# Kernel optimization log

Measured on AMD Instinct MI355X. Metric: run time of the kernel, lower is better.

The kernel has to match this reference:

```python
import jax, jax.numpy as jnp
import numpy as np

NUM_HEADS = 32
ROPE_THETA = 10000.0


def _apply_rope_neox(x, positions):
    # x: [B, S, H, D], positions: [B, S]
    D = x.shape[-1]
    inv_freq = 1.0 / (ROPE_THETA ** (jnp.arange(0, D, 2, dtype=jnp.float32) / D))  # [D/2]
    ang = positions.astype(jnp.float32)[..., None] * inv_freq  # [B, S, D/2]
    cos = jnp.cos(ang)[:, :, None, :]  # [B, S, 1, D/2]
    sin = jnp.sin(ang)[:, :, None, :]
    x1, x2 = x[..., : D // 2], x[..., D // 2 :]
    return jnp.concatenate([x1 * cos - x2 * sin, x2 * cos + x1 * sin], axis=-1)


def setup_inputs() -> dict:
    key = jax.random.key(0)
    ks = jax.random.split(key, 4)
    B, S, H = 2, 2048, 4096
    positions = jnp.broadcast_to(jnp.arange(S, dtype=jnp.int32), (B, S))
    hidden_states = jax.random.normal(ks[0], (B, S, H), dtype=jnp.float32)
    w_qkv = jax.random.normal(ks[1], (H, 3 * H), dtype=jnp.float32) * (H ** -0.5)
    b_qkv = jax.random.normal(ks[2], (3 * H,), dtype=jnp.float32) * 0.02
    w_proj = jax.random.normal(ks[3], (H, H), dtype=jnp.float32) * (H ** -0.5)
    return {"positions": positions, "hidden_states": hidden_states,
            "w_qkv": w_qkv, "b_qkv": b_qkv, "w_proj": w_proj}


def reference(positions, hidden_states, w_qkv, b_qkv, w_proj):
    B, S, H = hidden_states.shape
    nh = NUM_HEADS
    hd = H // nh
    scale = hd ** -0.5

    qkv = hidden_states @ w_qkv + b_qkv  # [B, S, 3H]
    q, k, v = jnp.split(qkv, 3, axis=-1)
    q = q.reshape(B, S, nh, hd)
    k = k.reshape(B, S, nh, hd)
    v = v.reshape(B, S, nh, hd)

    q = _apply_rope_neox(q, positions)
    k = _apply_rope_neox(k, positions)

    scores = jnp.einsum("bqhd,bkhd->bhqk", q, k) * scale  # [B, H, S, S]
    causal = jnp.tril(jnp.ones((S, S), dtype=bool))
    scores = jnp.where(causal, scores, jnp.finfo(scores.dtype).min)
    probs = jax.nn.softmax(scores, axis=-1)
    attn = jnp.einsum("bhqk,bkhd->bqhd", probs, v).reshape(B, S, H)

    return attn @ w_proj
```

## Files before the change

kernel.cpp:

```cpp
#include <hip/hip_runtime.h>

#define NHD 32
#define SS  2048
#define HH  4096
#define H3  12288
#define HD  128

typedef __attribute__((ext_vector_type(4))) float f32x4;
typedef __attribute__((ext_vector_type(8))) short short8;

#define GLOAD_LDS16(gptr, lptr)                                                        \
  __builtin_amdgcn_global_load_lds((const __attribute__((address_space(1))) void*)(gptr), \
                                   (__attribute__((address_space(3))) void*)(lptr), 16, 0, 0)

__device__ __forceinline__ ushort f2bf(float f) {
  union { float f; unsigned u; } v; v.f = f;
  unsigned r = (v.u + 0x7FFFu + ((v.u >> 16) & 1u)) >> 16;
  return (ushort)r;
}
__device__ __forceinline__ float bf2f(ushort u) {
  union { unsigned u; float f; } v; v.u = ((unsigned)u) << 16;
  return v.f;
}

__global__ __launch_bounds__(256) void cvt_f32_bf16(const float* __restrict__ in,
                                                    ushort* __restrict__ out) {
  size_t i = ((size_t)blockIdx.x * 256 + threadIdx.x) * 4;
  float4 v = *(const float4*)(in + i);
  ushort4 r; r.x = f2bf(v.x); r.y = f2bf(v.y); r.z = f2bf(v.z); r.w = f2bf(v.w);
  *(ushort4*)(out + i) = r;
}

__global__ __launch_bounds__(256) void transpose_cvt(const float* __restrict__ in,
                                                     ushort* __restrict__ out,
                                                     int rows, int cols) {
  __shared__ float tile[32][33];
  int c0 = blockIdx.x * 32, r0 = blockIdx.y * 32;
  int tx = threadIdx.x, ty = threadIdx.y;
  #pragma unroll
  for (int i = ty; i < 32; i += 8)
    tile[i][tx] = in[(size_t)(r0 + i) * cols + (c0 + tx)];
  __syncthreads();
  #pragma unroll
  for (int i = ty; i < 32; i += 8)
    out[(size_t)(c0 + i) * rows + (r0 + tx)] = f2bf(tile[tx][i]);
}

__global__ __launch_bounds__(256) void vtrans(const ushort* __restrict__ qkvb,
                                              ushort* __restrict__ vt) {
  __shared__ ushort tile[32][33];
  int s0 = blockIdx.x * 32, d0 = blockIdx.y * 32, bh = blockIdx.z;
  int b = bh >> 5, h = bh & 31;
  int tx = threadIdx.x, ty = threadIdx.y;
  #pragma unroll
  for (int i = ty; i < 32; i += 8)
    tile[i][tx] = qkvb[(size_t)(b * SS + s0 + i) * H3 + 8192 + h * 128 + d0 + tx];
  __syncthreads();
  #pragma unroll
  for (int i = ty; i < 32; i += 8)
    vt[((size_t)bh * HD + d0 + i) * SS + s0 + tx] = tile[tx][i];
}

template<bool BIAS, bool OUTBF16>
__global__ __launch_bounds__(256) void gemm_bf16(const ushort* __restrict__ A,
                                                 const ushort* __restrict__ BT,
                                                 const float* __restrict__ bias,
                                                 void* __restrict__ Cv,
                                                 int N, int K) {
  __shared__ __align__(16) ushort As[128 * 64];
  __shared__ __align__(16) ushort Bs[128 * 64];
  int tid  = threadIdx.x;
  int wave = tid >> 6, lane = tid & 63;
  int g = lane >> 4, q = lane & 15;
  int m0 = blockIdx.y * 128, n0 = blockIdx.x * 128;
  int wr = (wave >> 1) * 64, wc = (wave & 1) * 64;
  f32x4 acc[4][4] = {};
  for (int k0 = 0; k0 < K; k0 += 64) {
    __syncthreads();
    #pragma unroll
    for (int r = 0; r < 4; ++r) {
      int gr  = wave * 64 + 256 * r + lane;
      int row = gr >> 3, col = (gr & 7) << 3;
      int ldsbase = (wave * 64 + 256 * r) * 8;
      GLOAD_LDS16(A  + (size_t)(m0 + row) * K + k0 + col, &As[ldsbase]);
      GLOAD_LDS16(BT + (size_t)(n0 + row) * K + k0 + col, &Bs[ldsbase]);
    }
    __syncthreads();
    #pragma unroll
    for (int kk = 0; kk < 64; kk += 32) {
      short8 af[4], bfr[4];
      #pragma unroll
      for (int m = 0; m < 4; ++m)
        af[m] = *(const short8*)(&As[(wr + m * 16 + q) * 64 + kk + 8 * g]);
      #pragma unroll
      for (int n = 0; n < 4; ++n)
        bfr[n] = *(const short8*)(&Bs[(wc + n * 16 + q) * 64 + kk + 8 * g]);
      #pragma unroll
      for (int m = 0; m < 4; ++m)
        #pragma unroll
        for (int n = 0; n < 4; ++n)
          acc[m][n] = __builtin_amdgcn_mfma_f32_16x16x32_bf16(af[m], bfr[n], acc[m][n], 0, 0, 0);
    }
  }
  #pragma unroll
  for (int m = 0; m < 4; ++m) {
    #pragma unroll
    for (int n = 0; n < 4; ++n) {
      int gcol = n0 + wc + n * 16 + q;
      float bv = 0.f;
      if (BIAS) bv = bias[gcol];
      #pragma unroll
      for (int r = 0; r < 4; ++r) {
        int grow = m0 + wr + m * 16 + g * 4 + r;
        float v = acc[m][n][r] + bv;
        if (OUTBF16) ((ushort*)Cv)[(size_t)grow * N + gcol] = f2bf(v);
        else         ((float*) Cv)[(size_t)grow * N + gcol] = v;
      }
    }
  }
}

__global__ __launch_bounds__(256) void rope_split(const ushort* __restrict__ qkv,
                                                  const int* __restrict__ positions,
                                                  ushort* __restrict__ qb,
                                                  ushort* __restrict__ kb) {
  int id = blockIdx.x * 256 + threadIdx.x;
  int d = id & 63;
  int h = (id >> 6) & 31;
  int t = id >> 11;
  int b = t >> 11, s = t & 2047;
  float pos = (float)positions[t];
  float ang = pos * __expf(-(float)d * 0.14391156831212787f);
  float sv, cv;
  sincosf(ang, &sv, &cv);
  size_t src = (size_t)t * H3 + h * 128 + d;
  float q1 = bf2f(qkv[src]),        q2 = bf2f(qkv[src + 64]);
  float k1 = bf2f(qkv[src + 4096]), k2 = bf2f(qkv[src + 4160]);
  size_t dst = ((size_t)(b * NHD + h) * SS + s) * HD + d;
  qb[dst]      = f2bf(q1 * cv - q2 * sv);
  qb[dst + 64] = f2bf(q2 * cv + q1 * sv);
  kb[dst]      = f2bf(k1 * cv - k2 * sv);
  kb[dst + 64] = f2bf(k2 * cv + k1 * sv);
}

__global__ __launch_bounds__(256) void attn_fwd(const ushort* __restrict__ qb,
                                                const ushort* __restrict__ kb,
                                                const ushort* __restrict__ vt,
                                                ushort* __restrict__ aout) {
  __shared__ __align__(16) ushort Ks[64 * 128];
  __shared__ __align__(16) ushort Vs[128 * 64];
  __shared__ __align__(16) ushort Pw[4 * 32 * 68];
  const float SCALE = 0.08838834764831845f;
  int tid = threadIdx.x, wave = tid >> 6, lane = tid & 63;
  int g = lane >> 4, q = lane & 15;
  int swk = (q & 7) << 4;
  int bh = blockIdx.y;
  int qb0 = blockIdx.x * 128;
  const ushort* Qh = qb + (size_t)bh * SS * HD;
  const ushort* Kh = kb + (size_t)bh * SS * HD;
  const ushort* Vh = vt + (size_t)bh * SS * HD;
  ushort* Pm = &Pw[wave * 32 * 68];

  short8 qf[2][4];
  #pragma unroll
  for (int m = 0; m < 2; ++m)
    #pragma unroll
    for (int c = 0; c < 4; ++c)
      qf[m][c] = *(const short8*)(Qh + (size_t)(qb0 + wave * 32 + m * 16 + q) * HD + c * 32 + 8 * g);

  f32x4 o[2][8] = {};
  float mrow[2][4], lrow[2][4];
  #pragma unroll
  for (int m = 0; m < 2; ++m)
    #pragma unroll
    for (int r = 0; r < 4; ++r) { mrow[m][r] = -1e30f; lrow[m][r] = 0.f; }

  int nt = (qb0 >> 6) + 2;
  for (int kt = 0; kt < nt; ++kt) {
    int kv0 = kt * 64;
    __syncthreads();
    #pragma unroll
    for (int r = 0; r < 4; ++r) {
      int gi  = r * 256 + tid;
      int row = gi >> 4, xb = (gi & 15) << 4;
      int src = xb ^ ((row & 7) << 4);
      GLOAD_LDS16(Kh + (size_t)(kv0 + row) * HD + (src >> 1),
                  &Ks[(r * 256 + wave * 64) * 8]);
    }
    #pragma unroll
    for (int r = 0; r < 4; ++r) {
      int gi  = r * 256 + tid;
      int row = gi >> 3, xb = (gi & 7) << 4;
      int src = xb ^ ((row & 7) << 4);
      GLOAD_LDS16(Vh + (size_t)row * SS + kv0 + (src >> 1),
                  &Vs[(r * 256 + wave * 64) * 8]);
    }
    __syncthreads();

    f32x4 sf[2][4] = {};
    #pragma unroll
    for (int c = 0; c < 4; ++c) {
      #pragma unroll
      for (int n = 0; n < 4; ++n) {
        int row = n * 16 + q;
        short8 kf = *(const short8*)(&Ks[row * 128 + (((c * 64 + 16 * g) ^ swk) >> 1)]);
        #pragma unroll
        for (int m = 0; m < 2; ++m)
          sf[m][n] = __builtin_amdgcn_mfma_f32_16x16x32_bf16(qf[m][c], kf, sf[m][n], 0, 0, 0);
      }
    }

    bool masked = (kt >= nt - 2);
    float corr[2][4];
    #pragma unroll
    for (int m = 0; m < 2; ++m) {
      #pragma unroll
      for (int r = 0; r < 4; ++r) {
        int qrow = qb0 + wave * 32 + m * 16 + g * 4 + r;
        float x[4];
        #pragma unroll
        for (int n = 0; n < 4; ++n) {
          x[n] = sf[m][n][r] * SCALE;
          if (masked && (kv0 + n * 16 + q > qrow)) x[n] = -1e30f;
        }
        float mx = fmaxf(fmaxf(x[0], x[1]), fmaxf(x[2], x[3]));
        #pragma unroll
        for (int off = 8; off; off >>= 1) mx = fmaxf(mx, __shfl_xor(mx, off));
        float mnew = fmaxf(mrow[m][r], mx);
        corr[m][r] = __expf(mrow[m][r] - mnew);
        mrow[m][r] = mnew;
        float rs = 0.f;
        #pragma unroll
        for (int n = 0; n < 4; ++n) {
          float p = __expf(x[n] - mnew);
          rs += p;
          Pm[(m * 16 + g * 4 + r) * 68 + n * 16 + q] = f2bf(p);
        }
        #pragma unroll
        for (int off = 8; off; off >>= 1) rs += __shfl_xor(rs, off);
        lrow[m][r] = lrow[m][r] * corr[m][r] + rs;
      }
    }
    #pragma unroll
    for (int m = 0; m < 2; ++m)
      #pragma unroll
      for (int d0 = 0; d0 < 8; ++d0)
        #pragma unroll
        for (int r = 0; r < 4; ++r) o[m][d0][r] *= corr[m][r];

    short8 pf[2][2];
    #pragma unroll
    for (int m = 0; m < 2; ++m)
      #pragma unroll
      for (int c2 = 0; c2 < 2; ++c2)
        pf[m][c2] = *(const short8*)(&Pm[(m * 16 + q) * 68 + c2 * 32 + 8 * g]);
    #pragma unroll
    for (int d0 = 0; d0 < 8; ++d0) {
      int vrow = d0 * 16 + q;
      short8 vf0 = *(const short8*)(&Vs[vrow * 64 + (((16 * g) ^ swk) >> 1)]);
      short8 vf1 = *(const short8*)(&Vs[vrow * 64 + (((64 + 16 * g) ^ swk) >> 1)]);
      #pragma unroll
      for (int m = 0; m < 2; ++m) {
        o[m][d0] = __builtin_amdgcn_mfma_f32_16x16x32_bf16(pf[m][0], vf0, o[m][d0], 0, 0, 0);
        o[m][d0] = __builtin_amdgcn_mfma_f32_16x16x32_bf16(pf[m][1], vf1, o[m][d0], 0, 0, 0);
      }
    }
  }

  int b = bh >> 5, h = bh & 31;
  #pragma unroll
  for (int m = 0; m < 2; ++m) {
    #pragma unroll
    for (int r = 0; r < 4; ++r) {
      float inv = 1.0f / lrow[m][r];
      int srow = qb0 + wave * 32 + m * 16 + g * 4 + r;
      size_t base = ((size_t)(b * SS + srow)) * HH + h * 128;
      #pragma unroll
      for (int d0 = 0; d0 < 8; ++d0)
        aout[base + d0 * 16 + q] = f2bf(o[m][d0][r] * inv);
    }
  }
}

extern "C" void kernel_launch(void* const* d_in, const int* in_sizes, int n_in,
                              void* d_out, int out_size, void* d_ws, size_t ws_size,
                              hipStream_t stream) {
  const int*   positions = (const int*)  d_in[0];
  const float* hidden    = (const float*)d_in[1];
  const float* w_qkv     = (const float*)d_in[2];
  const float* b_qkv     = (const float*)d_in[3];
  const float* w_proj    = (const float*)d_in[4];
  float* out = (float*)d_out;

  char* ws = (char*)d_ws;
  ushort* hsb   = (ushort*)(ws);
  ushort* wqkvT = (ushort*)(ws + 0x02000000ULL);
  ushort* wpT   = (ushort*)(ws + 0x08000000ULL);
  ushort* qkvb  = (ushort*)(ws + 0x0A000000ULL);
  ushort* qbuf  = (ushort*)(ws + 0x10000000ULL);
  ushort* kbuf  = (ushort*)(ws + 0x12000000ULL);
  ushort* vtb   = (ushort*)(ws + 0x14000000ULL);
  ushort* aout  = hsb;

  cvt_f32_bf16<<<16384, 256, 0, stream>>>(hidden, hsb);
  transpose_cvt<<<dim3(384, 128), dim3(32, 8), 0, stream>>>(w_qkv, wqkvT, HH, H3);
  transpose_cvt<<<dim3(128, 128), dim3(32, 8), 0, stream>>>(w_proj, wpT, HH, HH);

  gemm_bf16<true, true><<<dim3(96, 32), 256, 0, stream>>>(hsb, wqkvT, b_qkv, qkvb, H3, HH);

  rope_split<<<32768, 256, 0, stream>>>(qkvb, positions, qbuf, kbuf);
  vtrans<<<dim3(64, 4, 64), dim3(32, 8), 0, stream>>>(qkvb, vtb);

  attn_fwd<<<dim3(16, 64), 256, 0, stream>>>(qbuf, kbuf, vtb, aout);

  gemm_bf16<false, false><<<dim3(32, 32), 256, 0, stream>>>(aout, wpT, nullptr, out, HH, HH);
}
```

Measured before the change: 1.744 ms.

## Replace GEMM with 256x256 double-buffered, swizzled, 8-wave pipelined kernel

Replaces the 128x128 single-buffered bf16 GEMM with a 256x256 tile kernel using 8 waves, double-buffered LDS, XOR-swizzled LDS layout, and interleaved async global-to-LDS loads with MFMA quadrants under raised wave priority. The aim is to hide global load latency behind MFMA work, avoid LDS bank conflicts, and raise arithmetic intensity per block. In exchange it uses 128KB of LDS per block and many more accumulator registers. The out-projection GEMM gets only 256 blocks, which may underfill the GPU.

```diff
diff --git a/kernel.cpp b/kernel.cpp
--- a/kernel.cpp
+++ b/kernel.cpp
@@ -62,57 +62,169 @@
 }
 
 template<bool BIAS, bool OUTBF16>
-__global__ __launch_bounds__(256) void gemm_bf16(const ushort* __restrict__ A,
-                                                 const ushort* __restrict__ BT,
-                                                 const float* __restrict__ bias,
-                                                 void* __restrict__ Cv,
-                                                 int N, int K) {
-  __shared__ __align__(16) ushort As[128 * 64];
-  __shared__ __align__(16) ushort Bs[128 * 64];
-  int tid  = threadIdx.x;
-  int wave = tid >> 6, lane = tid & 63;
-  int g = lane >> 4, q = lane & 15;
-  int m0 = blockIdx.y * 128, n0 = blockIdx.x * 128;
-  int wr = (wave >> 1) * 64, wc = (wave & 1) * 64;
-  f32x4 acc[4][4] = {};
-  for (int k0 = 0; k0 < K; k0 += 64) {
-    __syncthreads();
-    #pragma unroll
-    for (int r = 0; r < 4; ++r) {
-      int gr  = wave * 64 + 256 * r + lane;
-      int row = gr >> 3, col = (gr & 7) << 3;
-      int ldsbase = (wave * 64 + 256 * r) * 8;
-      GLOAD_LDS16(A  + (size_t)(m0 + row) * K + k0 + col, &As[ldsbase]);
-      GLOAD_LDS16(BT + (size_t)(n0 + row) * K + k0 + col, &Bs[ldsbase]);
-    }
-    __syncthreads();
-    #pragma unroll
-    for (int kk = 0; kk < 64; kk += 32) {
-      short8 af[4], bfr[4];
-      #pragma unroll
-      for (int m = 0; m < 4; ++m)
-        af[m] = *(const short8*)(&As[(wr + m * 16 + q) * 64 + kk + 8 * g]);
-      #pragma unroll
-      for (int n = 0; n < 4; ++n)
-        bfr[n] = *(const short8*)(&Bs[(wc + n * 16 + q) * 64 + kk + 8 * g]);
-      #pragma unroll
-      for (int m = 0; m < 4; ++m)
-        #pragma unroll
-        for (int n = 0; n < 4; ++n)
-          acc[m][n] = __builtin_amdgcn_mfma_f32_16x16x32_bf16(af[m], bfr[n], acc[m][n], 0, 0, 0);
-    }
-  }
-  #pragma unroll
-  for (int m = 0; m < 4; ++m) {
-    #pragma unroll
-    for (int n = 0; n < 4; ++n) {
-      int gcol = n0 + wc + n * 16 + q;
+__global__ __launch_bounds__(512, 2) void gemm256(const ushort* __restrict__ A,
+                                                  const ushort* __restrict__ BT,
+                                                  const float* __restrict__ bias,
+                                                  void* __restrict__ Cv,
+                                                  int N, int K) {
+  __shared__ __align__(16) ushort As_[2][256 * 64];
+  __shared__ __align__(16) ushort Bs_[2][256 * 64];
+  const int tid = threadIdx.x;
+  const int wave = tid >> 6, lane = tid & 63;
+  const int g = lane >> 4, q = lane & 15;
+  const int wm = wave >> 2, wn = wave & 3;
+  const int m0 = blockIdx.y * 256, n0 = blockIdx.x * 256;
+  const int NT = K >> 6;
+
+  int srow[2], scol[2], sbase[2];
+  #pragma unroll
+  for (int r = 0; r < 2; ++r) {
+    int gi = r * 512 + tid;
+    int row = gi >> 3, colb = (gi & 7) << 4;
+    srow[r] = row;
+    scol[r] = (colb ^ ((row & 7) << 4)) >> 1;
+    sbase[r] = (r * 512 + wave * 64) * 8;
+  }
+
+#define STG_A(p, h, t)                                                                   \
+  do {                                                                                   \
+    GLOAD_LDS16(A + (size_t)(m0 + (h) * 128 + srow[0]) * K + (t) * 64 + scol[0],         \
+                &As_[p][(h) * 8192 + sbase[0]]);                                         \
+    GLOAD_LDS16(A + (size_t)(m0 + (h) * 128 + srow[1]) * K + (t) * 64 + scol[1],         \
+                &As_[p][(h) * 8192 + sbase[1]]);                                         \
+  } while (0)
+#define STG_B(p, h, t)                                                                   \
+  do {                                                                                   \
+    GLOAD_LDS16(BT + (size_t)(n0 + (h) * 128 + srow[0]) * K + (t) * 64 + scol[0],        \
+                &Bs_[p][(h) * 8192 + sbase[0]]);                                         \
+    GLOAD_LDS16(BT + (size_t)(n0 + (h) * 128 + srow[1]) * K + (t) * 64 + scol[1],        \
+                &Bs_[p][(h) * 8192 + sbase[1]]);                                         \
+  } while (0)
+
+  int fcol[2];
+  #pragma unroll
+  for (int kk = 0; kk < 2; ++kk)
+    fcol[kk] = ((kk * 64 + 16 * g) ^ ((q & 7) << 4)) >> 1;
+
+  f32x4 acc[8][4] = {};
+  short8 af[4][2], bf[2][2][2];
+
+  STG_A(0, 0, 0); STG_A(0, 1, 0); STG_B(0, 0, 0); STG_B(0, 1, 0);
+  if (NT > 1) {
+    STG_A(1, 0, 1); STG_B(1, 0, 1);
+    asm volatile("s_waitcnt vmcnt(4)" ::: "memory");
+  } else {
+    asm volatile("s_waitcnt vmcnt(0)" ::: "memory");
+  }
+  __builtin_amdgcn_sched_barrier(0);
+  __syncthreads();
+
+  for (int t = 0; t < NT; ++t) {
+    const int p = t & 1;
+    const ushort* Ap = As_[p];
+    const ushort* Bp = Bs_[p];
+
+    #pragma unroll
+    for (int i = 0; i < 4; ++i) {
+      int row = wm * 128 + i * 16 + q;
+      af[i][0] = *(const short8*)(&Ap[row * 64 + fcol[0]]);
+      af[i][1] = *(const short8*)(&Ap[row * 64 + fcol[1]]);
+    }
+    #pragma unroll
+    for (int j = 0; j < 2; ++j) {
+      int row = wn * 64 + j * 16 + q;
+      bf[0][j][0] = *(const short8*)(&Bp[row * 64 + fcol[0]]);
+      bf[0][j][1] = *(const short8*)(&Bp[row * 64 + fcol[1]]);
+    }
+    if (t + 1 < NT) STG_A(p ^ 1, 1, t + 1);
+    __syncthreads();
+    asm volatile("s_waitcnt lgkmcnt(0)" ::: "memory");
+    __builtin_amdgcn_sched_barrier(0);
+    __builtin_amdgcn_s_setprio(1);
+    #pragma unroll
+    for (int i = 0; i < 4; ++i)
+      #pragma unroll
+      for (int j = 0; j < 2; ++j) {
+        acc[i][j] = __builtin_amdgcn_mfma_f32_16x16x32_bf16(af[i][0], bf[0][j][0], acc[i][j], 0, 0, 0);
+        acc[i][j] = __builtin_amdgcn_mfma_f32_16x16x32_bf16(af[i][1], bf[0][j][1], acc[i][j], 0, 0, 0);
+      }
+    __builtin_amdgcn_s_setprio(0);
+    __syncthreads();
+
+    #pragma unroll
+    for (int j = 0; j < 2; ++j) {
+      int row = wn * 64 + (2 + j) * 16 + q;
+      bf[1][j][0] = *(const short8*)(&Bp[row * 64 + fcol[0]]);
+      bf[1][j][1] = *(const short8*)(&Bp[row * 64 + fcol[1]]);
+    }
+    if (t + 1 < NT) STG_B(p ^ 1, 1, t + 1);
+    __syncthreads();
+    asm volatile("s_waitcnt lgkmcnt(0)" ::: "memory");
+    __builtin_amdgcn_sched_barrier(0);
+    __builtin_amdgcn_s_setprio(1);
+    #pragma unroll
+    for (int i = 0; i < 4; ++i)
+      #pragma unroll
+      for (int j = 0; j < 2; ++j) {
+        acc[i][2 + j] = __builtin_amdgcn_mfma_f32_16x16x32_bf16(af[i][0], bf[1][j][0], acc[i][2 + j], 0, 0, 0);
+        acc[i][2 + j] = __builtin_amdgcn_mfma_f32_16x16x32_bf16(af[i][1], bf[1][j][1], acc[i][2 + j], 0, 0, 0);
+      }
+    __builtin_amdgcn_s_setprio(0);
+    __syncthreads();
+
+    #pragma unroll
+    for (int i = 0; i < 4; ++i) {
+      int row = wm * 128 + 64 + i * 16 + q;
+      af[i][0] = *(const short8*)(&Ap[row * 64 + fcol[0]]);
+      af[i][1] = *(const short8*)(&Ap[row * 64 + fcol[1]]);
+    }
+    if (t + 2 < NT) STG_B(p, 0, t + 2);
+    __syncthreads();
+    asm volatile("s_waitcnt lgkmcnt(0)" ::: "memory");
+    __builtin_amdgcn_sched_barrier(0);
+    __builtin_amdgcn_s_setprio(1);
+    #pragma unroll
+    for (int i = 0; i < 4; ++i)
+      #pragma unroll
+      for (int j = 0; j < 2; ++j) {
+        acc[4 + i][j] = __builtin_amdgcn_mfma_f32_16x16x32_bf16(af[i][0], bf[0][j][0], acc[4 + i][j], 0, 0, 0);
+        acc[4 + i][j] = __builtin_amdgcn_mfma_f32_16x16x32_bf16(af[i][1], bf[0][j][1], acc[4 + i][j], 0, 0, 0);
+      }
+    __builtin_amdgcn_s_setprio(0);
+    __syncthreads();
+
+    if (t + 2 < NT) STG_A(p, 0, t + 2);
+    __syncthreads();
+    __builtin_amdgcn_s_setprio(1);
+    #pragma unroll
+    for (int i = 0; i < 4; ++i)
+      #pragma unroll
+      for (int j = 0; j < 2; ++j) {
+        acc[4 + i][2 + j] = __builtin_amdgcn_mfma_f32_16x16x32_bf16(af[i][0], bf[1][j][0], acc[4 + i][2 + j], 0, 0, 0);
+        acc[4 + i][2 + j] = __builtin_amdgcn_mfma_f32_16x16x32_bf16(af[i][1], bf[1][j][1], acc[4 + i][2 + j], 0, 0, 0);
+      }
+    __builtin_amdgcn_s_setprio(0);
+    if (t + 1 < NT) {
+      if (t + 2 < NT) asm volatile("s_waitcnt vmcnt(4)" ::: "memory");
+      else            asm volatile("s_waitcnt vmcnt(0)" ::: "memory");
+      __builtin_amdgcn_sched_barrier(0);
+    }
+    __syncthreads();
+  }
+#undef STG_A
+#undef STG_B
+
+  #pragma unroll
+  for (int mf = 0; mf < 8; ++mf) {
+    #pragma unroll
+    for (int nf = 0; nf < 4; ++nf) {
+      int gcol = n0 + wn * 64 + nf * 16 + q;
       float bv = 0.f;
       if (BIAS) bv = bias[gcol];
       #pragma unroll
       for (int r = 0; r < 4; ++r) {
-        int grow = m0 + wr + m * 16 + g * 4 + r;
-        float v = acc[m][n][r] + bv;
+        int grow = m0 + wm * 128 + mf * 16 + g * 4 + r;
+        float v = acc[mf][nf][r] + bv;
         if (OUTBF16) ((ushort*)Cv)[(size_t)grow * N + gcol] = f2bf(v);
         else         ((float*) Cv)[(size_t)grow * N + gcol] = v;
       }
@@ -306,12 +418,12 @@
   transpose_cvt<<<dim3(384, 128), dim3(32, 8), 0, stream>>>(w_qkv, wqkvT, HH, H3);
   transpose_cvt<<<dim3(128, 128), dim3(32, 8), 0, stream>>>(w_proj, wpT, HH, HH);
 
-  gemm_bf16<true, true><<<dim3(96, 32), 256, 0, stream>>>(hsb, wqkvT, b_qkv, qkvb, H3, HH);
+  gemm256<true, true><<<dim3(48, 16), 512, 0, stream>>>(hsb, wqkvT, b_qkv, qkvb, H3, HH);
 
   rope_split<<<32768, 256, 0, stream>>>(qkvb, positions, qbuf, kbuf);
   vtrans<<<dim3(64, 4, 64), dim3(32, 8), 0, stream>>>(qkvb, vtb);
 
   attn_fwd<<<dim3(16, 64), 256, 0, stream>>>(qbuf, kbuf, vtb, aout);
 
-  gemm_bf16<false, false><<<dim3(32, 32), 256, 0, stream>>>(aout, wpT, nullptr, out, HH, HH);
-}
+  gemm256<false, false><<<dim3(16, 16), 512, 0, stream>>>(aout, wpT, nullptr, out, HH, HH);
+}
```

New measurement: 1.815 ms. 1.04x slower.
